# Kernel tuning notes

Hardware: AMD Instinct MI355X
Metric: run time of the kernel (lower is better)

Reference implementation:

```python
import jax, jax.numpy as jnp
import numpy as np

DIM = 2048
NUM_HEADS = 16
NUM_KV_HEADS = 4
HEAD_DIM = DIM // NUM_HEADS  # 128
ROPE_DIMS = HEAD_DIM         # rope_dims=0 -> full head_dim
ROPE_BASE = 10000.0
EPS = jnp.finfo(jnp.float32).eps  # torch F.rms_norm default eps


def _rms_norm(x):
    # F.rms_norm over last dim, no learned weight
    return x * jax.lax.rsqrt(jnp.mean(x * x, axis=-1, keepdims=True) + EPS)


def _rope_cos_sin(seq_len, dtype):
    inv_freq = 1.0 / (ROPE_BASE ** (jnp.arange(0, ROPE_DIMS, 2, dtype=jnp.float32) / ROPE_DIMS))
    t = jnp.arange(seq_len, dtype=jnp.float32)
    freqs = jnp.outer(t, inv_freq)  # [S, rope_dims/2]
    return jnp.cos(freqs).astype(dtype), jnp.sin(freqs).astype(dtype)


def _apply_rotary(x, cos, sin):
    # x: [B, H, S, hd]; cos/sin: [S, rope_dims/2] broadcast over B,H
    half = ROPE_DIMS // 2
    x1, x2 = x[..., :half], x[..., half:ROPE_DIMS]
    x_pass = x[..., ROPE_DIMS:]
    rotated = jnp.concatenate((x1 * cos + x2 * sin, -x1 * sin + x2 * cos), axis=-1)
    return jnp.concatenate((rotated, x_pass), axis=-1) if x_pass.shape[-1] else rotated


def setup_inputs() -> dict:
    key = jax.random.key(0)
    ks = jax.random.split(key, 6)
    B, S = 2, 2048
    kv_dim = NUM_KV_HEADS * HEAD_DIM
    scale = 0.02
    return {
        "x": jax.random.normal(ks[0], (B, S, DIM), dtype=jnp.float32),
        "Wq": jax.random.normal(ks[1], (DIM, DIM), dtype=jnp.float32) * scale,
        "Wk": jax.random.normal(ks[2], (kv_dim, DIM), dtype=jnp.float32) * scale,
        "Wv": jax.random.normal(ks[3], (kv_dim, DIM), dtype=jnp.float32) * scale,
        "Wproj": jax.random.normal(ks[4], (DIM, DIM), dtype=jnp.float32) * scale,
        "q_gain": jnp.full((NUM_HEADS,), 1.0, dtype=jnp.float32),
    }


def reference(x, Wq, Wk, Wv, Wproj, q_gain):
    B, S, D = x.shape
    H, KV, hd = NUM_HEADS, NUM_KV_HEADS, HEAD_DIM
    group = H // KV

    # QKV projections (Linear: y = x @ W.T)
    q = (x @ Wq.T).reshape(B, S, H, hd).transpose(0, 2, 1, 3)    # [B,H,S,hd]
    k = (x @ Wk.T).reshape(B, S, KV, hd).transpose(0, 2, 1, 3)   # [B,KV,S,hd]
    v = (x @ Wv.T).reshape(B, S, KV, hd).transpose(0, 2, 1, 3)

    # Per-head RMSNorm on q/k
    q = _rms_norm(q)
    k = _rms_norm(k)

    # RoPE
    cos, sin = _rope_cos_sin(S, q.dtype)
    q = _apply_rotary(q, cos, sin)
    k = _apply_rotary(k, cos, sin)

    # Per-head gain on q
    q = q * q_gain[None, :, None, None]

    # GQA: expand kv heads to H
    k = jnp.repeat(k, group, axis=1)  # [B,H,S,hd]
    v = jnp.repeat(v, group, axis=1)

    # Causal SDPA
    sm_scale = 1.0 / np.sqrt(hd)
    scores = jnp.einsum('bhqd,bhkd->bhqk', q, k) * sm_scale
    causal = jnp.tril(jnp.ones((S, S), dtype=bool))
    scores = jnp.where(causal, scores, -jnp.inf)
    attn = jax.nn.softmax(scores, axis=-1)
    y = jnp.einsum('bhqk,bhkd->bhqd', attn, v)

    y = y.transpose(0, 2, 1, 3).reshape(B, S, D)
    return y @ Wproj.T
```

## Files before the change

kernel.cpp:

```cpp
#include <hip/hip_runtime.h>
#include <hip/hip_bf16.h>
#include <stdint.h>

namespace {

constexpr int kB = 2;
constexpr int kS = 2048;
constexpr int kD = 2048;
constexpr int kH = 16;
constexpr int kKV = 4;
constexpr int kHd = 128;
constexpr int kM = kB * kS;
constexpr int kQKN = kD + kKV * kHd;

using bf = __bf16;
typedef bf bf16x8 __attribute__((ext_vector_type(8)));
typedef float f32x4 __attribute__((ext_vector_type(4)));
typedef float f32x16 __attribute__((ext_vector_type(16)));

__device__ __forceinline__ f32x4 mfma16(bf16x8 a, bf16x8 b, f32x4 c) {
  return __builtin_amdgcn_mfma_f32_16x16x32_bf16(a, b, c, 0, 0, 0);
}
__device__ __forceinline__ f32x16 mfma32(bf16x8 a, bf16x8 b, f32x16 c) {
  return __builtin_amdgcn_mfma_f32_32x32x16_bf16(a, b, c, 0, 0, 0);
}

__device__ __forceinline__ void gload_lds16(const bf* g, bf* l) {
  __builtin_amdgcn_global_load_lds(
      (const __attribute__((address_space(1))) void*)(uintptr_t)g,
      (__attribute__((address_space(3))) void*)l, 16, 0, 0);
}

__global__ __launch_bounds__(256) void cvt_kernel(const float* __restrict__ src,
                                                  bf* __restrict__ dst, int n4) {
  int i = blockIdx.x * 256 + threadIdx.x;
  if (i >= n4) return;
  float4 v = reinterpret_cast<const float4*>(src)[i];
  union { bf h[4]; uint2 u; } o;
  o.h[0] = (bf)v.x; o.h[1] = (bf)v.y; o.h[2] = (bf)v.z; o.h[3] = (bf)v.w;
  reinterpret_cast<uint2*>(dst)[i] = o.u;
}

template <typename CT>
__global__ __launch_bounds__(256) void gemm_bt(const bf* __restrict__ A, int lda,
                                               const bf* __restrict__ Bm, int ldb,
                                               CT* __restrict__ C, int ldc, int K) {
  __shared__ bf As[128 * 64];
  __shared__ bf Bs[128 * 64];
  const int tid = threadIdx.x;
  const int w = tid >> 6, lane = tid & 63;
  const int r16 = lane & 15, kg = lane >> 4;
  const int nwg = gridDim.x * gridDim.y;
  const int bid = blockIdx.y * gridDim.x + blockIdx.x;
  const int swz = (bid & 7) * (nwg >> 3) + (bid >> 3);
  const int bx = swz % gridDim.x, by = swz / gridDim.x;
  const int bm = by * 128, bn = bx * 128;
  const int wy = (w >> 1) * 64, wx = (w & 1) * 64;
  f32x4 acc[4][4] = {};
  for (int kt = 0; kt < K; kt += 64) {
    __syncthreads();
#pragma unroll
    for (int r = 0; r < 4; r++) {
      int u = r * 256 + tid;
      int row = u >> 3;
      int cb = ((u & 7) * 16) ^ ((row & 7) << 4);
      gload_lds16(A + (size_t)(bm + row) * lda + kt + (cb >> 1),
                  As + (size_t)(r * 256 + w * 64) * 8);
      gload_lds16(Bm + (size_t)(bn + row) * ldb + kt + (cb >> 1),
                  Bs + (size_t)(r * 256 + w * 64) * 8);
    }
    __syncthreads();
#pragma unroll
    for (int ks = 0; ks < 2; ks++) {
      bf16x8 af[4], bfr[4];
#pragma unroll
      for (int m = 0; m < 4; m++) {
        int row = wy + m * 16 + r16;
        af[m] = *reinterpret_cast<const bf16x8*>(
            reinterpret_cast<const char*>(As) + row * 128 +
            ((ks * 64 + kg * 16) ^ ((row & 7) << 4)));
      }
#pragma unroll
      for (int n = 0; n < 4; n++) {
        int row = wx + n * 16 + r16;
        bfr[n] = *reinterpret_cast<const bf16x8*>(
            reinterpret_cast<const char*>(Bs) + row * 128 +
            ((ks * 64 + kg * 16) ^ ((row & 7) << 4)));
      }
#pragma unroll
      for (int m = 0; m < 4; m++)
#pragma unroll
        for (int n = 0; n < 4; n++)
          acc[m][n] = mfma16(af[m], bfr[n], acc[m][n]);
    }
  }
#pragma unroll
  for (int m = 0; m < 4; m++)
#pragma unroll
    for (int n = 0; n < 4; n++)
#pragma unroll
      for (int r = 0; r < 4; r++) {
        int row = bm + wy + m * 16 + kg * 4 + r;
        int col = bn + wx + n * 16 + r16;
        C[(size_t)row * ldc + col] = (CT)acc[m][n][r];
      }
}

__global__ __launch_bounds__(256) void normrope(bf* __restrict__ qk,
                                                const float* __restrict__ qgain) {
  const int tid = threadIdx.x;
  const int w = tid >> 6, lane = tid & 63;
  int v = blockIdx.x * 4 + w;
  int b = v / (kS * (kH + kKV));
  int rem = v % (kS * (kH + kKV));
  int s = rem / (kH + kKV);
  int j = rem % (kH + kKV);
  int colbase = (j < kH) ? j * kHd : kD + (j - kH) * kHd;
  size_t base = (size_t)(b * kS + s) * kQKN + colbase;
  float e1 = (float)qk[base + lane];
  float e2 = (float)qk[base + 64 + lane];
  float ss = e1 * e1 + e2 * e2;
#pragma unroll
  for (int m = 1; m < 64; m <<= 1) ss += __shfl_xor(ss, m);
  float inv = rsqrtf(ss * (1.0f / 128.0f) + 1.1920929e-7f);
  e1 *= inv; e2 *= inv;
  float invfreq = powf(10000.0f, -(float)lane * (1.0f / 64.0f));
  float ang = (float)s * invfreq;
  float sn, cs;
  sincosf(ang, &sn, &cs);
  float o1 = e1 * cs + e2 * sn;
  float o2 = -e1 * sn + e2 * cs;
  if (j < kH) {
    float g = qgain[j] * (0.08838834764831845f * 1.4426950408889634f);
    o1 *= g; o2 *= g;
  }
  qk[base + lane] = (bf)o1;
  qk[base + 64 + lane] = (bf)o2;
}

__global__ __launch_bounds__(256, 2) void attn_kernel(const bf* __restrict__ qk,
                                                      const bf* __restrict__ vt,
                                                      bf* __restrict__ y) {
  __shared__ bf Ks[2][64 * 128];
  __shared__ bf Vs[2][128 * 64];
  __shared__ float Ml[2][64][2];
  const int tid = threadIdx.x;
  const int w = tid >> 6, lane = tid & 63;
  const int q32 = lane & 31, hi = lane >> 5;
  const int qhalf = w & 1, kvhalf = w >> 1;
  const int bh = blockIdx.x;
  const int pairIdx = blockIdx.y;
  const int b = bh >> 4, h = bh & 15, kvh = h >> 2;
  const size_t rowbase = (size_t)b * kS;
  const bf* kbase = qk + kD + kvh * kHd;
  const bf* vbase = vt + (size_t)(kvh * kHd) * kM + b * kS;

  const bf* gK[4]; const bf* gV[4];
#pragma unroll
  for (int r = 0; r < 4; r++) {
    int u = r * 256 + tid;
    int krow = u >> 4, c16 = u & 15;
    gK[r] = kbase + (size_t)(rowbase + krow) * kQKN +
            (((c16 * 16) ^ ((krow & 7) << 4)) >> 1);
    int vrow = u >> 3, c8 = u & 7;
    gV[r] = vbase + (size_t)vrow * kM +
            (((c8 * 16) ^ ((vrow & 7) << 4)) >> 1);
  }

  auto stage = [&](int buf, int kt) {
    const size_t ko = (size_t)kt * (size_t)(64 * kQKN);
    const int vo = kt * 64;
#pragma unroll
    for (int r = 0; r < 4; r++)
      gload_lds16(gK[r] + ko, Ks[buf] + (size_t)(r * 256 + w * 64) * 8);
#pragma unroll
    for (int r = 0; r < 4; r++)
      gload_lds16(gV[r] + vo, Vs[buf] + (size_t)(r * 256 + w * 64) * 8);
  };

#pragma unroll 1
  for (int ph = 0; ph < 2; ph++) {
    const int j = ph ? (31 - pairIdx) : pairIdx;
    const int q0 = j * 64;
    const int qg0 = q0 + qhalf * 32;
    const int qrow = qg0 + q32;
    const int kvoff = kvhalf * 32;

    bf16x8 qf[8];
#pragma unroll
    for (int dc = 0; dc < 8; dc++)
      qf[dc] = *reinterpret_cast<const bf16x8*>(
          qk + (rowbase + qrow) * kQKN + h * kHd + dc * 16 + hi * 8);

    f32x16 o[4] = {};
    float mrun = -1e30f, lrun = 0.f;

    int cur = 0;
    stage(0, 0);

    for (int kt = 0; kt <= j; kt++) {
      asm volatile("s_barrier" ::: "memory");
      if (kt < j) {
        stage(cur ^ 1, kt + 1);
        asm volatile("s_waitcnt vmcnt(8)" ::: "memory");
      } else {
        asm volatile("s_waitcnt vmcnt(0)" ::: "memory");
      }
      asm volatile("s_barrier" ::: "memory");

      if (kt * 64 + kvoff <= qg0 + 31) {
        f32x16 sf = {};
        __builtin_amdgcn_s_setprio(1);
#pragma unroll
        for (int dc = 0; dc < 8; dc++) {
          int krow = kvoff + q32;
          bf16x8 kf = *reinterpret_cast<const bf16x8*>(
              reinterpret_cast<const char*>(Ks[cur]) + krow * 256 +
              ((dc * 32 + hi * 16) ^ ((krow & 7) << 4)));
          sf = mfma32(kf, qf[dc], sf);
        }
        __builtin_amdgcn_s_setprio(0);

        if (kt * 64 + kvoff + 31 > qg0) {
#pragma unroll
          for (int r = 0; r < 16; r++) {
            int kgl = kt * 64 + kvoff + (r & 3) + 8 * (r >> 2) + 4 * hi;
            sf[r] = (kgl <= qrow) ? sf[r] : -1e30f;
          }
        }

        float rmax = sf[0];
#pragma unroll
        for (int r = 1; r < 16; r++) rmax = fmaxf(rmax, sf[r]);
        rmax = fmaxf(rmax, __shfl_xor(rmax, 32));

        if (!__all(rmax <= mrun + 8.0f)) {
          float mnew = fmaxf(mrun, rmax);
          float resc = exp2f(mrun - mnew);
          mrun = mnew;
          lrun *= resc;
          float rq[16];
#pragma unroll
          for (int r = 0; r < 16; r++)
            rq[r] = __shfl(resc, (r & 3) + 8 * (r >> 2) + 4 * hi);
#pragma unroll
          for (int db = 0; db < 4; db++)
#pragma unroll
            for (int r = 0; r < 16; r++) o[db][r] *= rq[r];
        }

        float rsum = 0.f;
#pragma unroll
        for (int r = 0; r < 16; r++) {
          float p = exp2f(sf[r] - mrun);
          sf[r] = p;
          rsum += p;
        }
        rsum += __shfl_xor(rsum, 32);
        lrun += rsum;

        bf16x8 pa[2];
        {
          uint32_t wa[4], wb[4];
#pragma unroll
          for (int g = 0; g < 4; g++) {
            asm("v_cvt_pk_bf16_f32 %0, %1, %2"
                : "=v"(wa[g]) : "v"(sf[4 * g + 0]), "v"(sf[4 * g + 1]));
            asm("v_cvt_pk_bf16_f32 %0, %1, %2"
                : "=v"(wb[g]) : "v"(sf[4 * g + 2]), "v"(sf[4 * g + 3]));
          }
          asm volatile("v_permlane32_swap_b32 %0, %1" : "+v"(wa[0]), "+v"(wa[1]));
          asm volatile("v_permlane32_swap_b32 %0, %1" : "+v"(wb[0]), "+v"(wb[1]));
          asm volatile("v_permlane32_swap_b32 %0, %1" : "+v"(wa[2]), "+v"(wa[3]));
          asm volatile("v_permlane32_swap_b32 %0, %1" : "+v"(wb[2]), "+v"(wb[3]));
          union { uint32_t u[4]; bf16x8 v; } p0, p1;
          p0.u[0] = wa[0]; p0.u[1] = wb[0]; p0.u[2] = wa[1]; p0.u[3] = wb[1];
          p1.u[0] = wa[2]; p1.u[1] = wb[2]; p1.u[2] = wa[3]; p1.u[3] = wb[3];
          pa[0] = p0.v; pa[1] = p1.v;
        }

        __builtin_amdgcn_s_setprio(1);
#pragma unroll
        for (int c = 0; c < 2; c++)
#pragma unroll
          for (int db = 0; db < 4; db++) {
            int vrow = db * 32 + q32;
            bf16x8 vb = *reinterpret_cast<const bf16x8*>(
                reinterpret_cast<const char*>(Vs[cur]) + vrow * 128 +
                ((kvhalf * 64 + c * 32 + hi * 16) ^ ((vrow & 7) << 4)));
            o[db] = mfma32(pa[c], vb, o[db]);
          }
        __builtin_amdgcn_s_setprio(0);
      }
      cur ^= 1;
    }

    __syncthreads();
    float* mb = reinterpret_cast<float*>(Ks);
    if (w >= 2) {
      Ml[w - 2][lane][0] = mrun;
      Ml[w - 2][lane][1] = lrun;
      int base = (w - 2) * 4096;
#pragma unroll
      for (int db = 0; db < 4; db++)
#pragma unroll
        for (int r = 0; r < 16; r++)
          mb[base + (db * 16 + r) * 64 + lane] = o[db][r];
    }
    __syncthreads();
    if (w < 2) {
      float m1 = Ml[w][lane][0], l1 = Ml[w][lane][1];
      float m = fmaxf(mrun, m1);
      float f0 = exp2f(mrun - m), f1 = exp2f(m1 - m);
      float linv = 1.0f / (lrun * f0 + l1 * f1);
      float av = f0 * linv, bv = f1 * linv;
      float aq[16], bq[16];
#pragma unroll
      for (int r = 0; r < 16; r++) {
        int cr = (r & 3) + 8 * (r >> 2) + 4 * hi;
        aq[r] = __shfl(av, cr);
        bq[r] = __shfl(bv, cr);
      }
      int base = w * 4096;
#pragma unroll
      for (int db = 0; db < 4; db++)
#pragma unroll
        for (int r = 0; r < 16; r++) {
          float pv = mb[base + (db * 16 + r) * 64 + lane];
          float res = o[db][r] * aq[r] + pv * bq[r];
          int s = qg0 + (r & 3) + 8 * (r >> 2) + 4 * hi;
          int d = db * 32 + q32;
          y[(rowbase + s) * kD + h * kHd + d] = (bf)res;
        }
    }
    __syncthreads();
  }
}

}

extern "C" void kernel_launch(void* const* d_in, const int* in_sizes, int n_in,
                              void* d_out, int out_size, void* d_ws, size_t ws_size,
                              hipStream_t stream) {
  const float* x  = (const float*)d_in[0];
  const float* Wq = (const float*)d_in[1];
  const float* Wk = (const float*)d_in[2];
  const float* Wv = (const float*)d_in[3];
  const float* Wp = (const float*)d_in[4];
  const float* qg = (const float*)d_in[5];

  bf* xb    = (bf*)d_ws;
  bf* wqkvb = xb + (size_t)kM * kD;
  bf* wpb   = wqkvb + (size_t)3072 * kD;
  bf* qkbuf = wpb + (size_t)kD * kD;
  bf* vtbuf = qkbuf + (size_t)kM * kQKN;
  bf* yb    = vtbuf + (size_t)512 * kM;

  cvt_kernel<<<(kM * kD / 4) / 256, 256, 0, stream>>>(x, xb, kM * kD / 4);
  cvt_kernel<<<(kD * kD / 4) / 256, 256, 0, stream>>>(Wq, wqkvb, kD * kD / 4);
  cvt_kernel<<<(512 * kD / 4) / 256, 256, 0, stream>>>(Wk, wqkvb + (size_t)kD * kD, 512 * kD / 4);
  cvt_kernel<<<(512 * kD / 4) / 256, 256, 0, stream>>>(Wv, wqkvb + (size_t)kD * kD + (size_t)512 * kD, 512 * kD / 4);
  cvt_kernel<<<(kD * kD / 4) / 256, 256, 0, stream>>>(Wp, wpb, kD * kD / 4);

  gemm_bt<bf><<<dim3(kQKN / 128, kM / 128), 256, 0, stream>>>(xb, kD, wqkvb, kD, qkbuf, kQKN, kD);

  gemm_bt<bf><<<dim3(kM / 128, 512 / 128), 256, 0, stream>>>(
      wqkvb + (size_t)(kD + 512) * kD, kD, xb, kD, vtbuf, kM, kD);

  normrope<<<(kB * kS * (kH + kKV)) / 4, 256, 0, stream>>>(qkbuf, qg);

  attn_kernel<<<dim3(kB * kH, 16), 256, 0, stream>>>(qkbuf, vtbuf, yb);

  gemm_bt<float><<<dim3(kD / 128, kM / 128), 256, 0, stream>>>(yb, kD, wpb, kD, (float*)d_out, kD, kD);
}
```

Before: 248.7 us.

## Fuse conversion launches, shrink V-GEMM tile, split QK MFMA chains, use max3

Merges five fp32-to-bf16 conversion launches into one kernel so fewer launches are issued. Templates the GEMM on M-tile height and runs the V^T projection with 64-row tiles, giving 256 blocks instead of 128 to fill more CUs. In attention, splits the QK^T MFMA accumulation into two independent chains to shorten the dependency chain, and uses v_max3 for the row max. Replaces powf with exp2f for the RoPE frequency, which can change rounding slightly.

```diff
diff --git a/kernel.cpp b/kernel.cpp
--- a/kernel.cpp
+++ b/kernel.cpp
@@ -24,6 +24,11 @@
 __device__ __forceinline__ f32x16 mfma32(bf16x8 a, bf16x8 b, f32x16 c) {
   return __builtin_amdgcn_mfma_f32_32x32x16_bf16(a, b, c, 0, 0, 0);
 }
+__device__ __forceinline__ float max3f(float a, float b, float c) {
+  float d;
+  asm("v_max3_f32 %0, %1, %2, %3" : "=v"(d) : "v"(a), "v"(b), "v"(c));
+  return d;
+}
 
 __device__ __forceinline__ void gload_lds16(const bf* g, bf* l) {
   __builtin_amdgcn_global_load_lds(
@@ -31,21 +36,29 @@
       (__attribute__((address_space(3))) void*)l, 16, 0, 0);
 }
 
-__global__ __launch_bounds__(256) void cvt_kernel(const float* __restrict__ src,
-                                                  bf* __restrict__ dst, int n4) {
+__global__ __launch_bounds__(256) void cvt_all(
+    const float* __restrict__ x, const float* __restrict__ wq,
+    const float* __restrict__ wk, const float* __restrict__ wv,
+    const float* __restrict__ wp, bf* __restrict__ xb,
+    bf* __restrict__ wqkvb, bf* __restrict__ wpb) {
   int i = blockIdx.x * 256 + threadIdx.x;
-  if (i >= n4) return;
-  float4 v = reinterpret_cast<const float4*>(src)[i];
+  const float* src; bf* dst; int off;
+  if (i < 2097152)      { src = x;  dst = xb;    off = i; }
+  else if (i < 3145728) { src = wq; dst = wqkvb; off = i - 2097152; }
+  else if (i < 3407872) { src = wk; dst = wqkvb + (size_t)kD * kD;               off = i - 3145728; }
+  else if (i < 3670016) { src = wv; dst = wqkvb + (size_t)kD * kD + 512 * kD;    off = i - 3407872; }
+  else                  { src = wp; dst = wpb;   off = i - 3670016; }
+  float4 v = reinterpret_cast<const float4*>(src)[off];
   union { bf h[4]; uint2 u; } o;
   o.h[0] = (bf)v.x; o.h[1] = (bf)v.y; o.h[2] = (bf)v.z; o.h[3] = (bf)v.w;
-  reinterpret_cast<uint2*>(dst)[i] = o.u;
-}
-
-template <typename CT>
+  reinterpret_cast<uint2*>(dst)[off] = o.u;
+}
+
+template <typename CT, int TM>
 __global__ __launch_bounds__(256) void gemm_bt(const bf* __restrict__ A, int lda,
                                                const bf* __restrict__ Bm, int ldb,
                                                CT* __restrict__ C, int ldc, int K) {
-  __shared__ bf As[128 * 64];
+  __shared__ bf As[TM * 64];
   __shared__ bf Bs[128 * 64];
   const int tid = threadIdx.x;
   const int w = tid >> 6, lane = tid & 63;
@@ -54,27 +67,34 @@
   const int bid = blockIdx.y * gridDim.x + blockIdx.x;
   const int swz = (bid & 7) * (nwg >> 3) + (bid >> 3);
   const int bx = swz % gridDim.x, by = swz / gridDim.x;
-  const int bm = by * 128, bn = bx * 128;
-  const int wy = (w >> 1) * 64, wx = (w & 1) * 64;
-  f32x4 acc[4][4] = {};
+  const int bm = by * TM, bn = bx * 128;
+  const int wy = (w >> 1) * (TM / 2), wx = (w & 1) * 64;
+  constexpr int MF = TM / 32;
+  f32x4 acc[MF][4] = {};
   for (int kt = 0; kt < K; kt += 64) {
     __syncthreads();
 #pragma unroll
-    for (int r = 0; r < 4; r++) {
+    for (int r = 0; r < MF; r++) {
       int u = r * 256 + tid;
       int row = u >> 3;
       int cb = ((u & 7) * 16) ^ ((row & 7) << 4);
       gload_lds16(A + (size_t)(bm + row) * lda + kt + (cb >> 1),
                   As + (size_t)(r * 256 + w * 64) * 8);
+    }
+#pragma unroll
+    for (int r = 0; r < 4; r++) {
+      int u = r * 256 + tid;
+      int row = u >> 3;
+      int cb = ((u & 7) * 16) ^ ((row & 7) << 4);
       gload_lds16(Bm + (size_t)(bn + row) * ldb + kt + (cb >> 1),
                   Bs + (size_t)(r * 256 + w * 64) * 8);
     }
     __syncthreads();
 #pragma unroll
     for (int ks = 0; ks < 2; ks++) {
-      bf16x8 af[4], bfr[4];
-#pragma unroll
-      for (int m = 0; m < 4; m++) {
+      bf16x8 af[MF], bfr[4];
+#pragma unroll
+      for (int m = 0; m < MF; m++) {
         int row = wy + m * 16 + r16;
         af[m] = *reinterpret_cast<const bf16x8*>(
             reinterpret_cast<const char*>(As) + row * 128 +
@@ -88,14 +108,14 @@
             ((ks * 64 + kg * 16) ^ ((row & 7) << 4)));
       }
 #pragma unroll
-      for (int m = 0; m < 4; m++)
+      for (int m = 0; m < MF; m++)
 #pragma unroll
         for (int n = 0; n < 4; n++)
           acc[m][n] = mfma16(af[m], bfr[n], acc[m][n]);
     }
   }
 #pragma unroll
-  for (int m = 0; m < 4; m++)
+  for (int m = 0; m < MF; m++)
 #pragma unroll
     for (int n = 0; n < 4; n++)
 #pragma unroll
@@ -124,7 +144,7 @@
   for (int m = 1; m < 64; m <<= 1) ss += __shfl_xor(ss, m);
   float inv = rsqrtf(ss * (1.0f / 128.0f) + 1.1920929e-7f);
   e1 *= inv; e2 *= inv;
-  float invfreq = powf(10000.0f, -(float)lane * (1.0f / 64.0f));
+  float invfreq = exp2f((float)lane * -0.20762050593046013f);
   float ang = (float)s * invfreq;
   float sn, cs;
   sincosf(ang, &sn, &cs);
@@ -209,17 +229,22 @@
       asm volatile("s_barrier" ::: "memory");
 
       if (kt * 64 + kvoff <= qg0 + 31) {
-        f32x16 sf = {};
+        f32x16 sfA = {}, sfB = {};
+        const int krow = kvoff + q32;
+        const char* ksrow = reinterpret_cast<const char*>(Ks[cur]) + krow * 256;
+        const int kswz = (krow & 7) << 4;
         __builtin_amdgcn_s_setprio(1);
 #pragma unroll
-        for (int dc = 0; dc < 8; dc++) {
-          int krow = kvoff + q32;
-          bf16x8 kf = *reinterpret_cast<const bf16x8*>(
-              reinterpret_cast<const char*>(Ks[cur]) + krow * 256 +
-              ((dc * 32 + hi * 16) ^ ((krow & 7) << 4)));
-          sf = mfma32(kf, qf[dc], sf);
+        for (int dc = 0; dc < 4; dc++) {
+          bf16x8 kfA = *reinterpret_cast<const bf16x8*>(
+              ksrow + ((dc * 32 + hi * 16) ^ kswz));
+          bf16x8 kfB = *reinterpret_cast<const bf16x8*>(
+              ksrow + (((dc + 4) * 32 + hi * 16) ^ kswz));
+          sfA = mfma32(kfA, qf[dc], sfA);
+          sfB = mfma32(kfB, qf[dc + 4], sfB);
         }
         __builtin_amdgcn_s_setprio(0);
+        f32x16 sf = sfA + sfB;
 
         if (kt * 64 + kvoff + 31 > qg0) {
 #pragma unroll
@@ -229,9 +254,12 @@
           }
         }
 
-        float rmax = sf[0];
-#pragma unroll
-        for (int r = 1; r < 16; r++) rmax = fmaxf(rmax, sf[r]);
+        float t0 = max3f(sf[0], sf[1], sf[2]);
+        float t1 = max3f(sf[3], sf[4], sf[5]);
+        float t2 = max3f(sf[6], sf[7], sf[8]);
+        float t3 = max3f(sf[9], sf[10], sf[11]);
+        float t4 = max3f(sf[12], sf[13], sf[14]);
+        float rmax = fmaxf(max3f(t0, t1, t2), max3f(t3, t4, sf[15]));
         rmax = fmaxf(rmax, __shfl_xor(rmax, 32));
 
         if (!__all(rmax <= mrun + 8.0f)) {
@@ -356,20 +384,18 @@
   bf* vtbuf = qkbuf + (size_t)kM * kQKN;
   bf* yb    = vtbuf + (size_t)512 * kM;
 
-  cvt_kernel<<<(kM * kD / 4) / 256, 256, 0, stream>>>(x, xb, kM * kD / 4);
-  cvt_kernel<<<(kD * kD / 4) / 256, 256, 0, stream>>>(Wq, wqkvb, kD * kD / 4);
-  cvt_kernel<<<(512 * kD / 4) / 256, 256, 0, stream>>>(Wk, wqkvb + (size_t)kD * kD, 512 * kD / 4);
-  cvt_kernel<<<(512 * kD / 4) / 256, 256, 0, stream>>>(Wv, wqkvb + (size_t)kD * kD + (size_t)512 * kD, 512 * kD / 4);
-  cvt_kernel<<<(kD * kD / 4) / 256, 256, 0, stream>>>(Wp, wpb, kD * kD / 4);
-
-  gemm_bt<bf><<<dim3(kQKN / 128, kM / 128), 256, 0, stream>>>(xb, kD, wqkvb, kD, qkbuf, kQKN, kD);
-
-  gemm_bt<bf><<<dim3(kM / 128, 512 / 128), 256, 0, stream>>>(
+  cvt_all<<<18432, 256, 0, stream>>>(x, Wq, Wk, Wv, Wp, xb, wqkvb, wpb);
+
+  gemm_bt<bf, 128><<<dim3(kQKN / 128, kM / 128), 256, 0, stream>>>(
+      xb, kD, wqkvb, kD, qkbuf, kQKN, kD);
+
+  gemm_bt<bf, 64><<<dim3(kM / 128, 512 / 64), 256, 0, stream>>>(
       wqkvb + (size_t)(kD + 512) * kD, kD, xb, kD, vtbuf, kM, kD);
 
   normrope<<<(kB * kS * (kH + kKV)) / 4, 256, 0, stream>>>(qkbuf, qg);
 
   attn_kernel<<<dim3(kB * kH, 16), 256, 0, stream>>>(qkbuf, vtbuf, yb);
 
-  gemm_bt<float><<<dim3(kD / 128, kM / 128), 256, 0, stream>>>(yb, kD, wpb, kD, (float*)d_out, kD, kD);
-}
+  gemm_bt<float, 128><<<dim3(kD / 128, kM / 128), 256, 0, stream>>>(
+      yb, kD, wpb, kD, (float*)d_out, kD, kD);
+}
```

After: 226.2 us. -9.1%, faster.
